# Kernel tuning notes

Hardware: AMD Instinct MI355X
Metric: run time of the kernel (lower is better)

The kernel has to match this reference:

```python
import jax, jax.numpy as jnp
import numpy as np

N = 8192
F_IN = 256
F_OUT = 64
ALPHA = 0.2  # LeakyReLU negative slope
NEG_INF = -9e15


def setup_inputs() -> dict:
    key = jax.random.key(0)
    k1, k2, k3, k4 = jax.random.split(key, 4)
    h = jax.random.normal(k1, (N, F_IN), dtype=jnp.float32)
    adj = jax.random.randint(k2, (N, N), 0, 2, dtype=jnp.int32)
    W = jax.random.normal(k3, (F_IN, F_OUT), dtype=jnp.float32) * 0.1
    a = jax.random.normal(k4, (2 * F_OUT, 1), dtype=jnp.float32) * 0.1
    return {"h": h, "adj": adj, "W": W, "a": a}


def reference(h, adj, W, a):
    # Wh: [N, F_out]
    Wh = h @ W
    # e_ij = LeakyReLU(a1 . Wh_i + a2 . Wh_j); same math as the O(N^2*2F)
    # concat in the original, computed via two [N] gathers + broadcast add.
    f_src = Wh @ a[:F_OUT, 0]   # [N] contribution of node i (row)
    f_dst = Wh @ a[F_OUT:, 0]   # [N] contribution of node j (col)
    e = f_src[:, None] + f_dst[None, :]          # [N, N]
    e = jnp.where(e > 0, e, ALPHA * e)           # LeakyReLU
    # masked softmax over neighbors (dim=1)
    e = jnp.where(adj > 0, e, NEG_INF)
    attention = jax.nn.softmax(e, axis=1)        # [N, N]
    h_prime = attention @ Wh                     # [N, F_out]
    # concat=True -> ELU
    return jax.nn.elu(h_prime)
```

## Files before the change

### kernel.cpp

```cpp
#include <hip/hip_runtime.h>
#include <math.h>

#define N 8192
#define FIN 256
#define FOUT 64
#define ALPHA 0.2f
#define LOG2E 1.442695040888963f

#define JT 256
#define NTILE (N / JT)
#define ROWPITCH 512
#define ABUF (16 * ROWPITCH)
#define SMEM_BYTES (2 * ABUF)

typedef float f32x4 __attribute__((ext_vector_type(4)));
typedef _Float16 f16x8 __attribute__((ext_vector_type(8)));

union F16V { uint4 u; f16x8 h; };

__device__ __forceinline__ unsigned pack_f16(float a, float b) {
    union { _Float16 h; unsigned short u; } ca, cb;
    ca.h = (_Float16)a; cb.h = (_Float16)b;
    return (unsigned)ca.u | ((unsigned)cb.u << 16);
}
__device__ __forceinline__ float wcalc(int av, float fsr, float g) {
    float e = fsr + g;
    float le = e > 0.f ? e : ALPHA * e;
    float r = __builtin_exp2f(fmaf(le, LOG2E, -4.0f));
    return av != 0 ? r : 0.f;
}

__global__ __launch_bounds__(512) void gat_prep(
    const float* __restrict__ h, const float* __restrict__ W,
    const float* __restrict__ a,
    float* __restrict__ fsrc, float* __restrict__ fdst,
    uint4* __restrict__ Bp)
{
    __shared__ float sWh[32][FOUT + 1];
    const int t = threadIdx.x;
    const int f = t & 63;
    const int wq = t >> 6;
    const int row0 = blockIdx.x * 32;
    const int rbase = row0 + wq * 4;

    float acc[4] = {0.f, 0.f, 0.f, 0.f};
    for (int k0 = 0; k0 < FIN; k0 += 4) {
        const float w0 = W[(k0 + 0) * FOUT + f];
        const float w1 = W[(k0 + 1) * FOUT + f];
        const float w2 = W[(k0 + 2) * FOUT + f];
        const float w3 = W[(k0 + 3) * FOUT + f];
#pragma unroll
        for (int rr = 0; rr < 4; ++rr) {
            const float4 hv = *reinterpret_cast<const float4*>(
                &h[(size_t)(rbase + rr) * FIN + k0]);
            acc[rr] = fmaf(hv.x, w0, acc[rr]);
            acc[rr] = fmaf(hv.y, w1, acc[rr]);
            acc[rr] = fmaf(hv.z, w2, acc[rr]);
            acc[rr] = fmaf(hv.w, w3, acc[rr]);
        }
    }
    const float as = a[f], ad = a[FOUT + f];
#pragma unroll
    for (int rr = 0; rr < 4; ++rr) {
        sWh[wq * 4 + rr][f] = acc[rr];
        float fs = acc[rr] * as, fd = acc[rr] * ad;
#pragma unroll
        for (int off = 1; off < 64; off <<= 1) {
            fs += __shfl_xor(fs, off, 64);
            fd += __shfl_xor(fd, off, 64);
        }
        if (f == 0) { fsrc[rbase + rr] = fs; fdst[rbase + rr] = fd; }
    }
    __syncthreads();
    if (t < 256) {
        const int ft = t >> 6;
        const int l = t & 63;
        const int li = l & 15, g = l >> 4;
        float v[8];
#pragma unroll
        for (int e = 0; e < 8; ++e) v[e] = sWh[g * 8 + e][ft * 16 + li];
        uint4 pk;
        pk.x = pack_f16(v[0], v[1]);
        pk.y = pack_f16(v[2], v[3]);
        pk.z = pack_f16(v[4], v[5]);
        pk.w = pack_f16(v[6], v[7]);
        Bp[(size_t)(blockIdx.x * 4 + ft) * 64 + l] = pk;
    }
}

struct AdjG { int4 a0, a1; float4 g0, g1; };

__global__ __launch_bounds__(512, 4) void gat_main(
    const int* __restrict__ adj,
    const uint4* __restrict__ Bp,
    const float* __restrict__ fsrc, const float* __restrict__ fdst,
    float* __restrict__ out)
{
    __shared__ __align__(16) char smem[SMEM_BYTES];

    const int t = threadIdx.x;
    const int l = t & 63;
    const int w = t >> 6;
    const int row0 = blockIdx.x * 16;

    const int srow = t >> 5;
    const int sc8 = (t & 31) * 8;
    const float fsr = fsrc[row0 + srow];
    const size_t adjrow = (size_t)(row0 + srow) * N;
    const int awo = srow * ROWPITCH + (((t & 31) * 16) ^ ((srow & 7) << 4));

    const int ft = w & 3;
    const int p = w >> 2;
    const int r16 = l & 15;
    const int kg8 = (l >> 4) << 3;
    const int fswz = (r16 & 7) << 4;
    const int aro = r16 * ROWPITCH;
    const uint4* Bq = Bp + (size_t)p * 1024 + ft * 64 + l;

    f32x4 acc = {0.f, 0.f, 0.f, 0.f};
    float zacc = 0.f;
    AdjG AG;
    uint4 BA0, BA1, BA2, BA3, BB0, BB1, BB2, BB3;

#define BAR                                                                    \
    {                                                                          \
        asm volatile("s_waitcnt lgkmcnt(0)" ::: "memory");                     \
        __builtin_amdgcn_s_barrier();                                          \
    }

#define LOAD_ADJG(tile)                                                        \
    {                                                                          \
        const int j0_ = (tile) * JT;                                           \
        AG.a0 = *reinterpret_cast<const int4*>(&adj[adjrow + j0_ + sc8]);      \
        AG.a1 = *reinterpret_cast<const int4*>(&adj[adjrow + j0_ + sc8 + 4]);  \
        AG.g0 = *reinterpret_cast<const float4*>(&fdst[j0_ + sc8]);            \
        AG.g1 = *reinterpret_cast<const float4*>(&fdst[j0_ + sc8 + 4]);        \
    }

#define LOAD_B(tile, B0, B1, B2, B3)                                           \
    {                                                                          \
        const uint4* bq_ = Bq + (size_t)(tile) * 2048;                         \
        B0 = bq_[0];                                                           \
        B1 = bq_[256];                                                         \
        B2 = bq_[512];                                                         \
        B3 = bq_[768];                                                         \
    }

#define STAGE(BUF)                                                             \
    {                                                                          \
        const float w0 = wcalc(AG.a0.x, fsr, AG.g0.x);                         \
        const float w1 = wcalc(AG.a0.y, fsr, AG.g0.y);                         \
        const float w2 = wcalc(AG.a0.z, fsr, AG.g0.z);                         \
        const float w3 = wcalc(AG.a0.w, fsr, AG.g0.w);                         \
        const float w4 = wcalc(AG.a1.x, fsr, AG.g1.x);                         \
        const float w5 = wcalc(AG.a1.y, fsr, AG.g1.y);                         \
        const float w6 = wcalc(AG.a1.z, fsr, AG.g1.z);                         \
        const float w7 = wcalc(AG.a1.w, fsr, AG.g1.w);                         \
        zacc += (w0 + w1) + (w2 + w3) + ((w4 + w5) + (w6 + w7));               \
        uint4 pk;                                                              \
        pk.x = pack_f16(w0, w1); pk.y = pack_f16(w2, w3);                      \
        pk.z = pack_f16(w4, w5); pk.w = pack_f16(w6, w7);                      \
        *reinterpret_cast<uint4*>(smem + (BUF) * ABUF + awo) = pk;             \
    }

#define MFMA_PHASE(BUF, B0, B1, B2, B3)                                        \
    {                                                                          \
        const char* ab_ = smem + (BUF) * ABUF + aro;                           \
        F16V a0v, a1v, a2v, a3v, b0v, b1v, b2v, b3v;                           \
        a0v.u = *reinterpret_cast<const uint4*>(ab_ + (((p * 128 + 0 * 32 + kg8) * 2) ^ fswz)); \
        a1v.u = *reinterpret_cast<const uint4*>(ab_ + (((p * 128 + 1 * 32 + kg8) * 2) ^ fswz)); \
        a2v.u = *reinterpret_cast<const uint4*>(ab_ + (((p * 128 + 2 * 32 + kg8) * 2) ^ fswz)); \
        a3v.u = *reinterpret_cast<const uint4*>(ab_ + (((p * 128 + 3 * 32 + kg8) * 2) ^ fswz)); \
        b0v.u = B0; b1v.u = B1; b2v.u = B2; b3v.u = B3;                        \
        __builtin_amdgcn_s_setprio(1);                                         \
        acc = __builtin_amdgcn_mfma_f32_16x16x32_f16(a0v.h, b0v.h, acc, 0, 0, 0); \
        acc = __builtin_amdgcn_mfma_f32_16x16x32_f16(a1v.h, b1v.h, acc, 0, 0, 0); \
        acc = __builtin_amdgcn_mfma_f32_16x16x32_f16(a2v.h, b2v.h, acc, 0, 0, 0); \
        acc = __builtin_amdgcn_mfma_f32_16x16x32_f16(a3v.h, b3v.h, acc, 0, 0, 0); \
        __builtin_amdgcn_s_setprio(0);                                         \
    }

    LOAD_ADJG(0);
    LOAD_B(0, BA0, BA1, BA2, BA3);
    STAGE(0);
    LOAD_ADJG(1);
    BAR;

    for (int tt = 0; tt < NTILE; tt += 2) {
        if (tt + 1 < NTILE) LOAD_B(tt + 1, BB0, BB1, BB2, BB3);
        MFMA_PHASE(0, BA0, BA1, BA2, BA3);
        {
            STAGE(1);
            if (tt + 2 < NTILE) LOAD_ADJG(tt + 2);
        }
        BAR;
        if (tt + 2 < NTILE) LOAD_B(tt + 2, BA0, BA1, BA2, BA3);
        MFMA_PHASE(1, BB0, BB1, BB2, BB3);
        if (tt + 2 < NTILE) {
            STAGE(0);
            if (tt + 3 < NTILE) LOAD_ADJG(tt + 3);
        }
        BAR;
    }
#undef LOAD_ADJG
#undef LOAD_B
#undef STAGE
#undef MFMA_PHASE
#undef BAR

    __syncthreads();

    float* zb = reinterpret_cast<float*>(smem + 8192);
    {
        float z = zacc;
#pragma unroll
        for (int off = 1; off < 32; off <<= 1) z += __shfl_xor(z, off, 64);
        if ((l & 31) == 0) zb[srow] = z;
    }
    *reinterpret_cast<f32x4*>(smem + w * 1024 + l * 16) = acc;
    __syncthreads();
#pragma unroll
    for (int e0 = 0; e0 < 2; ++e0) {
        const int e = t + e0 * 512;
        const int rr = e >> 6, f2 = e & 63;
        const int ft2 = f2 >> 4, n = f2 & 15;
        const int ln = n | ((rr >> 2) << 4);
        const int rg = rr & 3;
        const float s =
            *reinterpret_cast<const float*>(smem + ft2 * 1024 + ln * 16 + rg * 4) +
            *reinterpret_cast<const float*>(smem + (ft2 + 4) * 1024 + ln * 16 + rg * 4);
        const float hp = s / zb[rr];
        out[(size_t)(row0 + rr) * FOUT + f2] = hp > 0.f ? hp : expm1f(hp);
    }
}

extern "C" void kernel_launch(void* const* d_in, const int* in_sizes, int n_in,
                              void* d_out, int out_size, void* d_ws, size_t ws_size,
                              hipStream_t stream) {
    const float* h   = (const float*)d_in[0];
    const int*   adj = (const int*)d_in[1];
    const float* W   = (const float*)d_in[2];
    const float* a   = (const float*)d_in[3];
    float* out = (float*)d_out;

    float* ws = (float*)d_ws;
    float* fsrc = ws;
    float* fdst = fsrc + N;
    uint4* Bp = (uint4*)(fdst + N);

    gat_prep<<<dim3(N / 32), dim3(512), 0, stream>>>(h, W, a, fsrc, fdst, Bp);
    gat_main<<<dim3(N / 16), dim3(512), 0, stream>>>(adj, Bp, fsrc, fdst, out);
}
```

Measured before the change: 91.67 us.

## Split attention columns across two blocks per row tile with separate reduce kernel

The main kernel now splits each 16-row tile's neighbour range into two halves handled by separate 256-thread blocks. Each wave covers one feature tile over the full 256-column K step with 8 MFMAs, instead of two waves splitting K. Partial accumulators and softmax denominators go to workspace, and a new reduce kernel combines the halves and applies the normalisation and ELU. The aim is more, smaller blocks for better occupancy and latency hiding, at the cost of an extra launch and partial-sum traffic through global memory.

```diff
diff --git a/kernel.cpp b/kernel.cpp
--- a/kernel.cpp
+++ b/kernel.cpp
@@ -7,10 +7,8 @@
 #define ALPHA 0.2f
 #define LOG2E 1.442695040888963f
 
-#define JT 256
-#define NTILE (N / JT)
-#define ROWPITCH 512
-#define ABUF (16 * ROWPITCH)
+#define NTH 16
+#define ABUF 8192
 #define SMEM_BYTES (2 * ABUF)
 
 typedef float f32x4 __attribute__((ext_vector_type(4)));
@@ -88,39 +86,40 @@
     }
 }
 
-struct AdjG { int4 a0, a1; float4 g0, g1; };
-
-__global__ __launch_bounds__(512, 4) void gat_main(
+__global__ __launch_bounds__(256, 4) void gat_main(
     const int* __restrict__ adj,
     const uint4* __restrict__ Bp,
     const float* __restrict__ fsrc, const float* __restrict__ fdst,
-    float* __restrict__ out)
+    f32x4* __restrict__ pacc, float* __restrict__ pz)
 {
     __shared__ __align__(16) char smem[SMEM_BYTES];
 
     const int t = threadIdx.x;
     const int l = t & 63;
     const int w = t >> 6;
-    const int row0 = blockIdx.x * 16;
-
-    const int srow = t >> 5;
-    const int sc8 = (t & 31) * 8;
+    const int rt = blockIdx.x >> 1;
+    const int hf = blockIdx.x & 1;
+    const int row0 = rt * 16;
+    const int jbase = hf * 4096;
+
+    const int srow = t >> 4;
+    const int scol = (t & 15) * 16;
     const float fsr = fsrc[row0 + srow];
-    const size_t adjrow = (size_t)(row0 + srow) * N;
-    const int awo = srow * ROWPITCH + (((t & 31) * 16) ^ ((srow & 7) << 4));
-
-    const int ft = w & 3;
-    const int p = w >> 2;
+    const size_t adjrow = (size_t)(row0 + srow) * N + jbase;
+    const int swz = (srow & 7) << 4;
+    const int awo0 = srow * 512 + ((scol * 2) ^ swz);
+    const int awo1 = srow * 512 + ((scol * 2 + 16) ^ swz);
+
     const int r16 = l & 15;
     const int kg8 = (l >> 4) << 3;
     const int fswz = (r16 & 7) << 4;
-    const int aro = r16 * ROWPITCH;
-    const uint4* Bq = Bp + (size_t)p * 1024 + ft * 64 + l;
+    const int aro = r16 * 512;
+    const uint4* Bq = Bp + (size_t)hf * 16 * 2048 + w * 64 + l;
 
     f32x4 acc = {0.f, 0.f, 0.f, 0.f};
     float zacc = 0.f;
-    AdjG AG;
-    uint4 BA0, BA1, BA2, BA3, BB0, BB1, BB2, BB3;
+    int4 A0, A1, A2, A3; float4 G0, G1, G2, G3;
+    uint4 B0, B1, B2, B3, B4, B5, B6, B7;
 
 #define BAR                                                                    \
     {                                                                          \
@@ -130,77 +129,85 @@
 
 #define LOAD_ADJG(tile)                                                        \
     {                                                                          \
-        const int j0_ = (tile) * JT;                                           \
-        AG.a0 = *reinterpret_cast<const int4*>(&adj[adjrow + j0_ + sc8]);      \
-        AG.a1 = *reinterpret_cast<const int4*>(&adj[adjrow + j0_ + sc8 + 4]);  \
-        AG.g0 = *reinterpret_cast<const float4*>(&fdst[j0_ + sc8]);            \
-        AG.g1 = *reinterpret_cast<const float4*>(&fdst[j0_ + sc8 + 4]);        \
-    }
-
-#define LOAD_B(tile, B0, B1, B2, B3)                                           \
+        const size_t o_ = adjrow + (tile) * 256 + scol;                        \
+        A0 = *reinterpret_cast<const int4*>(&adj[o_]);                         \
+        A1 = *reinterpret_cast<const int4*>(&adj[o_ + 4]);                     \
+        A2 = *reinterpret_cast<const int4*>(&adj[o_ + 8]);                     \
+        A3 = *reinterpret_cast<const int4*>(&adj[o_ + 12]);                    \
+        const int g_ = jbase + (tile) * 256 + scol;                            \
+        G0 = *reinterpret_cast<const float4*>(&fdst[g_]);                      \
+        G1 = *reinterpret_cast<const float4*>(&fdst[g_ + 4]);                  \
+        G2 = *reinterpret_cast<const float4*>(&fdst[g_ + 8]);                  \
+        G3 = *reinterpret_cast<const float4*>(&fdst[g_ + 12]);                 \
+    }
+
+#define LOAD_B(tile)                                                           \
     {                                                                          \
         const uint4* bq_ = Bq + (size_t)(tile) * 2048;                         \
-        B0 = bq_[0];                                                           \
-        B1 = bq_[256];                                                         \
-        B2 = bq_[512];                                                         \
-        B3 = bq_[768];                                                         \
+        B0 = bq_[0];    B1 = bq_[256];  B2 = bq_[512];  B3 = bq_[768];         \
+        B4 = bq_[1024]; B5 = bq_[1280]; B6 = bq_[1536]; B7 = bq_[1792];        \
     }
 
 #define STAGE(BUF)                                                             \
     {                                                                          \
-        const float w0 = wcalc(AG.a0.x, fsr, AG.g0.x);                         \
-        const float w1 = wcalc(AG.a0.y, fsr, AG.g0.y);                         \
-        const float w2 = wcalc(AG.a0.z, fsr, AG.g0.z);                         \
-        const float w3 = wcalc(AG.a0.w, fsr, AG.g0.w);                         \
-        const float w4 = wcalc(AG.a1.x, fsr, AG.g1.x);                         \
-        const float w5 = wcalc(AG.a1.y, fsr, AG.g1.y);                         \
-        const float w6 = wcalc(AG.a1.z, fsr, AG.g1.z);                         \
-        const float w7 = wcalc(AG.a1.w, fsr, AG.g1.w);                         \
-        zacc += (w0 + w1) + (w2 + w3) + ((w4 + w5) + (w6 + w7));               \
-        uint4 pk;                                                              \
-        pk.x = pack_f16(w0, w1); pk.y = pack_f16(w2, w3);                      \
-        pk.z = pack_f16(w4, w5); pk.w = pack_f16(w6, w7);                      \
-        *reinterpret_cast<uint4*>(smem + (BUF) * ABUF + awo) = pk;             \
-    }
-
-#define MFMA_PHASE(BUF, B0, B1, B2, B3)                                        \
+        float wv[16];                                                          \
+        wv[0] = wcalc(A0.x, fsr, G0.x);  wv[1] = wcalc(A0.y, fsr, G0.y);       \
+        wv[2] = wcalc(A0.z, fsr, G0.z);  wv[3] = wcalc(A0.w, fsr, G0.w);       \
+        wv[4] = wcalc(A1.x, fsr, G1.x);  wv[5] = wcalc(A1.y, fsr, G1.y);       \
+        wv[6] = wcalc(A1.z, fsr, G1.z);  wv[7] = wcalc(A1.w, fsr, G1.w);       \
+        wv[8] = wcalc(A2.x, fsr, G2.x);  wv[9] = wcalc(A2.y, fsr, G2.y);       \
+        wv[10] = wcalc(A2.z, fsr, G2.z); wv[11] = wcalc(A2.w, fsr, G2.w);      \
+        wv[12] = wcalc(A3.x, fsr, G3.x); wv[13] = wcalc(A3.y, fsr, G3.y);      \
+        wv[14] = wcalc(A3.z, fsr, G3.z); wv[15] = wcalc(A3.w, fsr, G3.w);      \
+        zacc += ((wv[0]+wv[1])+(wv[2]+wv[3])) + ((wv[4]+wv[5])+(wv[6]+wv[7]))  \
+              + ((wv[8]+wv[9])+(wv[10]+wv[11]))+((wv[12]+wv[13])+(wv[14]+wv[15])); \
+        uint4 p0, p1;                                                          \
+        p0.x = pack_f16(wv[0], wv[1]);   p0.y = pack_f16(wv[2], wv[3]);        \
+        p0.z = pack_f16(wv[4], wv[5]);   p0.w = pack_f16(wv[6], wv[7]);        \
+        p1.x = pack_f16(wv[8], wv[9]);   p1.y = pack_f16(wv[10], wv[11]);      \
+        p1.z = pack_f16(wv[12], wv[13]); p1.w = pack_f16(wv[14], wv[15]);      \
+        *reinterpret_cast<uint4*>(smem + (BUF) * ABUF + awo0) = p0;            \
+        *reinterpret_cast<uint4*>(smem + (BUF) * ABUF + awo1) = p1;            \
+    }
+
+#define MFMA_PHASE(BUF)                                                        \
     {                                                                          \
         const char* ab_ = smem + (BUF) * ABUF + aro;                           \
-        F16V a0v, a1v, a2v, a3v, b0v, b1v, b2v, b3v;                           \
-        a0v.u = *reinterpret_cast<const uint4*>(ab_ + (((p * 128 + 0 * 32 + kg8) * 2) ^ fswz)); \
-        a1v.u = *reinterpret_cast<const uint4*>(ab_ + (((p * 128 + 1 * 32 + kg8) * 2) ^ fswz)); \
-        a2v.u = *reinterpret_cast<const uint4*>(ab_ + (((p * 128 + 2 * 32 + kg8) * 2) ^ fswz)); \
-        a3v.u = *reinterpret_cast<const uint4*>(ab_ + (((p * 128 + 3 * 32 + kg8) * 2) ^ fswz)); \
-        b0v.u = B0; b1v.u = B1; b2v.u = B2; b3v.u = B3;                        \
         __builtin_amdgcn_s_setprio(1);                                         \
-        acc = __builtin_amdgcn_mfma_f32_16x16x32_f16(a0v.h, b0v.h, acc, 0, 0, 0); \
-        acc = __builtin_amdgcn_mfma_f32_16x16x32_f16(a1v.h, b1v.h, acc, 0, 0, 0); \
-        acc = __builtin_amdgcn_mfma_f32_16x16x32_f16(a2v.h, b2v.h, acc, 0, 0, 0); \
-        acc = __builtin_amdgcn_mfma_f32_16x16x32_f16(a3v.h, b3v.h, acc, 0, 0, 0); \
+        F16V a_, b_;                                                           \
+        a_.u = *reinterpret_cast<const uint4*>(ab_ + (((0*32 + kg8) * 2) ^ fswz)); \
+        b_.u = B0; acc = __builtin_amdgcn_mfma_f32_16x16x32_f16(a_.h, b_.h, acc, 0, 0, 0); \
+        a_.u = *reinterpret_cast<const uint4*>(ab_ + (((1*32 + kg8) * 2) ^ fswz)); \
+        b_.u = B1; acc = __builtin_amdgcn_mfma_f32_16x16x32_f16(a_.h, b_.h, acc, 0, 0, 0); \
+        a_.u = *reinterpret_cast<const uint4*>(ab_ + (((2*32 + kg8) * 2) ^ fswz)); \
+        b_.u = B2; acc = __builtin_amdgcn_mfma_f32_16x16x32_f16(a_.h, b_.h, acc, 0, 0, 0); \
+        a_.u = *reinterpret_cast<const uint4*>(ab_ + (((3*32 + kg8) * 2) ^ fswz)); \
+        b_.u = B3; acc = __builtin_amdgcn_mfma_f32_16x16x32_f16(a_.h, b_.h, acc, 0, 0, 0); \
+        a_.u = *reinterpret_cast<const uint4*>(ab_ + (((4*32 + kg8) * 2) ^ fswz)); \
+        b_.u = B4; acc = __builtin_amdgcn_mfma_f32_16x16x32_f16(a_.h, b_.h, acc, 0, 0, 0); \
+        a_.u = *reinterpret_cast<const uint4*>(ab_ + (((5*32 + kg8) * 2) ^ fswz)); \
+        b_.u = B5; acc = __builtin_amdgcn_mfma_f32_16x16x32_f16(a_.h, b_.h, acc, 0, 0, 0); \
+        a_.u = *reinterpret_cast<const uint4*>(ab_ + (((6*32 + kg8) * 2) ^ fswz)); \
+        b_.u = B6; acc = __builtin_amdgcn_mfma_f32_16x16x32_f16(a_.h, b_.h, acc, 0, 0, 0); \
+        a_.u = *reinterpret_cast<const uint4*>(ab_ + (((7*32 + kg8) * 2) ^ fswz)); \
+        b_.u = B7; acc = __builtin_amdgcn_mfma_f32_16x16x32_f16(a_.h, b_.h, acc, 0, 0, 0); \
         __builtin_amdgcn_s_setprio(0);                                         \
     }
 
     LOAD_ADJG(0);
-    LOAD_B(0, BA0, BA1, BA2, BA3);
-    STAGE(0);
-    LOAD_ADJG(1);
-    BAR;
-
-    for (int tt = 0; tt < NTILE; tt += 2) {
-        if (tt + 1 < NTILE) LOAD_B(tt + 1, BB0, BB1, BB2, BB3);
-        MFMA_PHASE(0, BA0, BA1, BA2, BA3);
-        {
-            STAGE(1);
-            if (tt + 2 < NTILE) LOAD_ADJG(tt + 2);
-        }
+    LOAD_B(0);
+
+    for (int tt = 0; tt < NTH; tt += 2) {
+        STAGE(0);
+        LOAD_ADJG(tt + 1);
         BAR;
-        if (tt + 2 < NTILE) LOAD_B(tt + 2, BA0, BA1, BA2, BA3);
-        MFMA_PHASE(1, BB0, BB1, BB2, BB3);
-        if (tt + 2 < NTILE) {
-            STAGE(0);
-            if (tt + 3 < NTILE) LOAD_ADJG(tt + 3);
-        }
+        MFMA_PHASE(0);
+        LOAD_B(tt + 1);
+        STAGE(1);
+        if (tt + 2 < NTH) LOAD_ADJG(tt + 2);
         BAR;
+        MFMA_PHASE(1);
+        if (tt + 2 < NTH) LOAD_B(tt + 2);
     }
 #undef LOAD_ADJG
 #undef LOAD_B
@@ -208,30 +215,32 @@
 #undef MFMA_PHASE
 #undef BAR
 
-    __syncthreads();
-
-    float* zb = reinterpret_cast<float*>(smem + 8192);
     {
         float z = zacc;
-#pragma unroll
-        for (int off = 1; off < 32; off <<= 1) z += __shfl_xor(z, off, 64);
-        if ((l & 31) == 0) zb[srow] = z;
-    }
-    *reinterpret_cast<f32x4*>(smem + w * 1024 + l * 16) = acc;
-    __syncthreads();
-#pragma unroll
-    for (int e0 = 0; e0 < 2; ++e0) {
-        const int e = t + e0 * 512;
-        const int rr = e >> 6, f2 = e & 63;
-        const int ft2 = f2 >> 4, n = f2 & 15;
-        const int ln = n | ((rr >> 2) << 4);
-        const int rg = rr & 3;
-        const float s =
-            *reinterpret_cast<const float*>(smem + ft2 * 1024 + ln * 16 + rg * 4) +
-            *reinterpret_cast<const float*>(smem + (ft2 + 4) * 1024 + ln * 16 + rg * 4);
-        const float hp = s / zb[rr];
-        out[(size_t)(row0 + rr) * FOUT + f2] = hp > 0.f ? hp : expm1f(hp);
-    }
+        z += __shfl_xor(z, 1, 64);
+        z += __shfl_xor(z, 2, 64);
+        z += __shfl_xor(z, 4, 64);
+        z += __shfl_xor(z, 8, 64);
+        if ((t & 15) == 0) pz[blockIdx.x * 16 + srow] = z;
+    }
+    pacc[(size_t)blockIdx.x * 256 + t] = acc;
+}
+
+__global__ __launch_bounds__(256) void gat_reduce(
+    const float* __restrict__ pacc, const float* __restrict__ pz,
+    float* __restrict__ out)
+{
+    const int e = blockIdx.x * 256 + threadIdx.x;
+    const int rt = e >> 10;
+    const int wi = e & 1023;
+    const int row = wi >> 6;
+    const int col = wi & 63;
+    const int idx = ((col >> 4) << 8) + ((row >> 2) << 6) + ((col & 15) << 2) + (row & 3);
+    const float s = pacc[(size_t)(rt * 2) * 1024 + idx] +
+                    pacc[(size_t)(rt * 2 + 1) * 1024 + idx];
+    const float z = pz[(rt * 2) * 16 + row] + pz[(rt * 2 + 1) * 16 + row];
+    const float hp = s / z;
+    out[(size_t)(rt * 16 + row) * 64 + col] = hp > 0.f ? hp : expm1f(hp);
 }
 
 extern "C" void kernel_launch(void* const* d_in, const int* in_sizes, int n_in,
@@ -247,7 +256,11 @@
     float* fsrc = ws;
     float* fdst = fsrc + N;
     uint4* Bp = (uint4*)(fdst + N);
+    float* paccf = (float*)(Bp + 65536);
+    float* pz = paccf + 1024 * 1024;
 
     gat_prep<<<dim3(N / 32), dim3(512), 0, stream>>>(h, W, a, fsrc, fdst, Bp);
-    gat_main<<<dim3(N / 16), dim3(512), 0, stream>>>(adj, Bp, fsrc, fdst, out);
-}
+    gat_main<<<dim3(1024), dim3(256), 0, stream>>>(
+        adj, Bp, fsrc, fdst, (f32x4*)paccf, pz);
+    gat_reduce<<<dim3(2048), dim3(256), 0, stream>>>(paccf, pz, out);
+}
```

Result: slower. 110.3 us (+20.3%).
